# Performance work log

Hardware: AMD Instinct MI355X
Metric: run time of the kernel (lower is better)

## Reference

```python
import jax, jax.numpy as jnp
import numpy as np
import math

N_EMBD = 1024
N_HEAD = 16
BLOCK = 2048
B, T = 2, 2048


def setup_inputs() -> dict:
    key = jax.random.key(0)
    ks = jax.random.split(key, 5)
    s = 0.02
    return {
        "x": jax.random.normal(ks[0], (B, T, N_EMBD), dtype=jnp.float32),
        "W_attn": jax.random.normal(ks[1], (3 * N_EMBD, N_EMBD), dtype=jnp.float32) * s,  # [out,in] torch layout
        "b_attn": jax.random.normal(ks[2], (3 * N_EMBD,), dtype=jnp.float32) * s,
        "W_proj": jax.random.normal(ks[3], (N_EMBD, N_EMBD), dtype=jnp.float32) * s,
        "b_proj": jax.random.normal(ks[4], (N_EMBD,), dtype=jnp.float32) * s,
    }


def reference(x, W_attn, b_attn, W_proj, b_proj):
    Bx, Tx, C = x.shape
    H = N_HEAD
    D = C // H
    qkv = jnp.einsum("btc,oc->bto", x, W_attn) + b_attn  # [B,T,3C]
    q, k, v = jnp.split(qkv, 3, axis=-1)
    # [B,T,H,D] -> [B,H,T,D]
    q = q.reshape(Bx, Tx, H, D).transpose(0, 2, 1, 3)
    k = k.reshape(Bx, Tx, H, D).transpose(0, 2, 1, 3)
    v = v.reshape(Bx, Tx, H, D).transpose(0, 2, 1, 3)
    att = jnp.einsum("bhqd,bhkd->bhqk", q, k) * (1.0 / math.sqrt(D))
    causal = jnp.tril(jnp.ones((Tx, Tx), dtype=bool))
    att = jnp.where(causal[None, None], att, -jnp.inf)
    att = jax.nn.softmax(att, axis=-1)
    y = jnp.einsum("bhqk,bhkd->bhqd", att, v)  # [B,H,T,D]
    y = y.transpose(0, 2, 1, 3).reshape(Bx, Tx, C)
    y = jnp.einsum("btc,oc->bto", y, W_proj) + b_proj
    return y
```

## Files before the change

### kernel.cpp

```cpp
#include <hip/hip_runtime.h>
#include <hip/hip_bf16.h>
#include <stdint.h>

typedef unsigned short u16;
using f32x4 = __attribute__((ext_vector_type(4))) float;
using s16x8 = __attribute__((ext_vector_type(8))) short;

#define B_SZ 2
#define T_SZ 2048
#define C_SZ 1024
#define H_SZ 16
#define D_SZ 64

#define Q_SCALE 0.18033688011112042f

__device__ __forceinline__ u16 f2bf(float f) {
  __hip_bfloat16 h = __float2bfloat16(f);
  return *(u16*)&h;
}

__device__ __forceinline__ void async16(const u16* g, u16* l) {
  __builtin_amdgcn_global_load_lds((__attribute__((address_space(1))) void*)(g),
                                   (__attribute__((address_space(3))) void*)(l),
                                   16, 0, 0);
}

__global__ void cvt3_kernel(const float* __restrict__ a, int na,
                            const float* __restrict__ b, int nb,
                            const float* __restrict__ c, int nc,
                            u16* __restrict__ out) {
  int n = na + nb + nc;
  for (int i = blockIdx.x * blockDim.x + threadIdx.x; i < n; i += gridDim.x * blockDim.x) {
    const float* src; int off;
    if (i < na)           { src = a; off = i; }
    else if (i < na + nb) { src = b; off = i - na; }
    else                  { src = c; off = i - na - nb; }
    float4 v = reinterpret_cast<const float4*>(src)[off];
    ushort4 o;
    o.x = f2bf(v.x); o.y = f2bf(v.y); o.z = f2bf(v.z); o.w = f2bf(v.w);
    reinterpret_cast<ushort4*>(out)[i] = o;
  }
}

__global__ __launch_bounds__(256) void gemm_qkv(
    const u16* __restrict__ A, const u16* __restrict__ W,
    const float* __restrict__ bias,
    u16* __restrict__ Qo, u16* __restrict__ Ko, u16* __restrict__ Vt)
{
  const int K = 1024;
  const int NT = 32;
  __shared__ __align__(16) u16 lA[2][128 * 32];
  __shared__ __align__(16) u16 lB[2][128 * 32];
  int tid = threadIdx.x, lane = tid & 63, wave = tid >> 6;
  int wm = (wave >> 1) * 64, wn = (wave & 1) * 64;
  int bm = blockIdx.x * 128, bn = blockIdx.y * 128;
  int r = lane & 15, g = lane >> 4;

  int p0 = tid, p1 = 256 + tid;
  int ar0 = p0 >> 2, ar1 = p1 >> 2;
  int al0 = (p0 & 3) ^ (ar0 & 3), al1 = (p1 & 3) ^ (ar1 & 3);
  const u16* As0 = A + (size_t)(bm + ar0) * K + al0 * 8;
  const u16* As1 = A + (size_t)(bm + ar1) * K + al1 * 8;
  const u16* Ws0 = W + (size_t)(bn + ar0) * K + al0 * 8;
  const u16* Ws1 = W + (size_t)(bn + ar1) * K + al1 * 8;

  f32x4 acc[4][4];
#pragma unroll
  for (int i = 0; i < 4; ++i)
#pragma unroll
    for (int j = 0; j < 4; ++j)
      acc[i][j] = (f32x4){0.f, 0.f, 0.f, 0.f};

  int rd_off = r * 32 + ((g ^ (r & 3)) * 8);

  async16(As0, &lA[0][p0 * 8]);
  async16(As1, &lA[0][p1 * 8]);
  async16(Ws0, &lB[0][p0 * 8]);
  async16(Ws1, &lB[0][p1 * 8]);
  __syncthreads();

  int cur = 0;
  for (int t = 0; t < NT; ++t) {
    if (t + 1 < NT) {
      int k0 = (t + 1) * 32;
      int nb_ = cur ^ 1;
      async16(As0 + k0, &lA[nb_][p0 * 8]);
      async16(As1 + k0, &lA[nb_][p1 * 8]);
      async16(Ws0 + k0, &lB[nb_][p0 * 8]);
      async16(Ws1 + k0, &lB[nb_][p1 * 8]);
    }
    s16x8 af[4], bf[4];
#pragma unroll
    for (int i = 0; i < 4; ++i)
      af[i] = *(const s16x8*)(&lA[cur][(wm + i * 16) * 32 + rd_off]);
#pragma unroll
    for (int j = 0; j < 4; ++j)
      bf[j] = *(const s16x8*)(&lB[cur][(wn + j * 16) * 32 + rd_off]);
#pragma unroll
    for (int i = 0; i < 4; ++i)
#pragma unroll
      for (int j = 0; j < 4; ++j)
        acc[i][j] = __builtin_amdgcn_mfma_f32_16x16x32_bf16(af[i], bf[j], acc[i][j], 0, 0, 0);
    __syncthreads();
    cur ^= 1;
  }

  int seg = bn >> 10;
#pragma unroll
  for (int i = 0; i < 4; ++i) {
#pragma unroll
    for (int j = 0; j < 4; ++j) {
      int col = bn + wn + j * 16 + r;
      int cc = col & 1023;
      int h = cc >> 6, d = cc & 63;
      float bv = bias[col];
      int row0 = bm + wm + i * 16 + g * 4;
      int b = row0 >> 11, t0 = row0 & 2047;
      if (seg == 2) {
        ushort4 pv;
        pv.x = f2bf(acc[i][j][0] + bv);
        pv.y = f2bf(acc[i][j][1] + bv);
        pv.z = f2bf(acc[i][j][2] + bv);
        pv.w = f2bf(acc[i][j][3] + bv);
        *reinterpret_cast<ushort4*>(Vt + ((size_t)(b * H_SZ + h) * D_SZ + d) * T_SZ + t0) = pv;
      } else {
        u16* dst = (seg == 0) ? Qo : Ko;
        float scale = (seg == 0) ? Q_SCALE : 1.0f;
#pragma unroll
        for (int rr = 0; rr < 4; ++rr) {
          float v = (acc[i][j][rr] + bv) * scale;
          dst[(((size_t)(b * H_SZ + h) * T_SZ + (t0 + rr)) * D_SZ) + d] = f2bf(v);
        }
      }
    }
  }
}

__global__ __launch_bounds__(256) void gemm_proj(
    const u16* __restrict__ A, const u16* __restrict__ W,
    const float* __restrict__ bias, float* __restrict__ out)
{
  const int K = 1024;
  const int NT = 32;
  __shared__ __align__(16) u16 lA[2][128 * 32];
  __shared__ __align__(16) u16 lB[2][128 * 32];
  int tid = threadIdx.x, lane = tid & 63, wave = tid >> 6;
  int wm = (wave >> 1) * 64, wn = (wave & 1) * 64;
  int bm = blockIdx.x * 128, bn = blockIdx.y * 128;
  int r = lane & 15, g = lane >> 4;

  int p0 = tid, p1 = 256 + tid;
  int ar0 = p0 >> 2, ar1 = p1 >> 2;
  int al0 = (p0 & 3) ^ (ar0 & 3), al1 = (p1 & 3) ^ (ar1 & 3);
  const u16* As0 = A + (size_t)(bm + ar0) * K + al0 * 8;
  const u16* As1 = A + (size_t)(bm + ar1) * K + al1 * 8;
  const u16* Ws0 = W + (size_t)(bn + ar0) * K + al0 * 8;
  const u16* Ws1 = W + (size_t)(bn + ar1) * K + al1 * 8;

  f32x4 acc[4][4];
#pragma unroll
  for (int i = 0; i < 4; ++i)
#pragma unroll
    for (int j = 0; j < 4; ++j)
      acc[i][j] = (f32x4){0.f, 0.f, 0.f, 0.f};

  int rd_off = r * 32 + ((g ^ (r & 3)) * 8);

  async16(As0, &lA[0][p0 * 8]);
  async16(As1, &lA[0][p1 * 8]);
  async16(Ws0, &lB[0][p0 * 8]);
  async16(Ws1, &lB[0][p1 * 8]);
  __syncthreads();

  int cur = 0;
  for (int t = 0; t < NT; ++t) {
    if (t + 1 < NT) {
      int k0 = (t + 1) * 32;
      int nb_ = cur ^ 1;
      async16(As0 + k0, &lA[nb_][p0 * 8]);
      async16(As1 + k0, &lA[nb_][p1 * 8]);
      async16(Ws0 + k0, &lB[nb_][p0 * 8]);
      async16(Ws1 + k0, &lB[nb_][p1 * 8]);
    }
    s16x8 af[4], bf[4];
#pragma unroll
    for (int i = 0; i < 4; ++i)
      af[i] = *(const s16x8*)(&lA[cur][(wm + i * 16) * 32 + rd_off]);
#pragma unroll
    for (int j = 0; j < 4; ++j)
      bf[j] = *(const s16x8*)(&lB[cur][(wn + j * 16) * 32 + rd_off]);
#pragma unroll
    for (int i = 0; i < 4; ++i)
#pragma unroll
      for (int j = 0; j < 4; ++j)
        acc[i][j] = __builtin_amdgcn_mfma_f32_16x16x32_bf16(af[i], bf[j], acc[i][j], 0, 0, 0);
    __syncthreads();
    cur ^= 1;
  }

#pragma unroll
  for (int i = 0; i < 4; ++i) {
#pragma unroll
    for (int j = 0; j < 4; ++j) {
      int col = bn + wn + j * 16 + r;
      float bv = bias[col];
#pragma unroll
      for (int rr = 0; rr < 4; ++rr) {
        int row = bm + wm + i * 16 + g * 4 + rr;
        out[(size_t)row * 1024 + col] = acc[i][j][rr] + bv;
      }
    }
  }
}

__global__ __launch_bounds__(256) void attn_kernel(
    const u16* __restrict__ Q, const u16* __restrict__ K, const u16* __restrict__ Vt,
    u16* __restrict__ Y)
{
  __shared__ __align__(16) u16 lK[2][64 * 64];
  __shared__ __align__(16) u16 lV[2][64 * 64];
  __shared__ __align__(16) u16 lP[4][16 * 64];
  int tid = threadIdx.x, lane = tid & 63, wave = tid >> 6;
  int bh = blockIdx.x;
  int qt = 31 - blockIdx.y;
  const u16* Qh = Q + (size_t)bh * T_SZ * D_SZ;
  const u16* Kh = K + (size_t)bh * T_SZ * D_SZ;
  const u16* Vh = Vt + (size_t)bh * D_SZ * T_SZ;
  int r = lane & 15, g = lane >> 4;
  int wq = qt * 64 + wave * 16;
  int qrow = wq + r;

  s16x8 qf0 = *(const s16x8*)(Qh + (size_t)qrow * 64 + g * 8);
  s16x8 qf1 = *(const s16x8*)(Qh + (size_t)qrow * 64 + 32 + g * 8);

  int p0 = tid, p1 = 256 + tid;
  int r0 = p0 >> 3, r1 = p1 >> 3;
  int l0 = (p0 & 7) ^ (r0 & 7), l1 = (p1 & 7) ^ (r1 & 7);

  float s0 = 0.f, s1 = 0.f, s2 = 0.f, s3 = 0.f;
  f32x4 o[4];
#pragma unroll
  for (int j = 0; j < 4; ++j) o[j] = (f32x4){0.f, 0.f, 0.f, 0.f};

  u16* lPw = lP[wave];

  async16(Kh + (size_t)r0 * 64 + l0 * 8, &lK[0][p0 * 8]);
  async16(Kh + (size_t)r1 * 64 + l1 * 8, &lK[0][p1 * 8]);
  async16(Vh + (size_t)r0 * T_SZ + l0 * 8, &lV[0][p0 * 8]);
  async16(Vh + (size_t)r1 * T_SZ + l1 * 8, &lV[0][p1 * 8]);
  __syncthreads();

  int cur = 0;
  for (int kt = 0; kt <= qt; ++kt) {
    int kvbase = kt * 64;
    if (kt < qt) {
      int nb_ = cur ^ 1;
      int kb = kvbase + 64;
      async16(Kh + (size_t)(kb + r0) * 64 + l0 * 8, &lK[nb_][p0 * 8]);
      async16(Kh + (size_t)(kb + r1) * 64 + l1 * 8, &lK[nb_][p1 * 8]);
      async16(Vh + (size_t)r0 * T_SZ + kb + l0 * 8, &lV[nb_][p0 * 8]);
      async16(Vh + (size_t)r1 * T_SZ + kb + l1 * 8, &lV[nb_][p1 * 8]);
    }

    f32x4 sf[4];
    __builtin_amdgcn_s_setprio(1);
#pragma unroll
    for (int jj = 0; jj < 4; ++jj) {
      int krow = jj * 16 + r;
      const s16x8 kf0 = *(const s16x8*)(&lK[cur][krow * 64 + ((g ^ (r & 7)) * 8)]);
      const s16x8 kf1 = *(const s16x8*)(&lK[cur][krow * 64 + (((4 + g) ^ (r & 7)) * 8)]);
      f32x4 sv = (f32x4){0.f, 0.f, 0.f, 0.f};
      sv = __builtin_amdgcn_mfma_f32_16x16x32_bf16(kf0, qf0, sv, 0, 0, 0);
      sv = __builtin_amdgcn_mfma_f32_16x16x32_bf16(kf1, qf1, sv, 0, 0, 0);
      sf[jj] = sv;
    }
    __builtin_amdgcn_s_setprio(0);

    if (kt == qt) {
#pragma unroll
      for (int jj = 0; jj < 4; ++jj)
#pragma unroll
        for (int rr = 0; rr < 4; ++rr) {
          int kv = kvbase + jj * 16 + g * 4 + rr;
          sf[jj][rr] = (kv <= qrow) ? sf[jj][rr] : -3e30f;
        }
    }

#pragma unroll
    for (int jj = 0; jj < 4; ++jj) {
      float pv0 = __builtin_amdgcn_exp2f(sf[jj][0]);
      float pv1 = __builtin_amdgcn_exp2f(sf[jj][1]);
      float pv2 = __builtin_amdgcn_exp2f(sf[jj][2]);
      float pv3 = __builtin_amdgcn_exp2f(sf[jj][3]);
      s0 += pv0; s1 += pv1; s2 += pv2; s3 += pv3;
      ushort4 pk;
      pk.x = f2bf(pv0); pk.y = f2bf(pv1); pk.z = f2bf(pv2); pk.w = f2bf(pv3);
      int off = r * 64 + ((jj * 16 + 4 * g) ^ ((r & 7) << 3));
      *reinterpret_cast<ushort4*>(lPw + off) = pk;
    }

    __builtin_amdgcn_s_setprio(1);
#pragma unroll
    for (int hh = 0; hh < 2; ++hh) {
      const s16x8 pa = *(const s16x8*)(lPw + r * 64 + (((hh * 4 + g) ^ (r & 7)) * 8));
#pragma unroll
      for (int j = 0; j < 4; ++j) {
        int vrow = j * 16 + r;
        const s16x8 vb = *(const s16x8*)(&lV[cur][vrow * 64 + (((hh * 4 + g) ^ (r & 7)) * 8)]);
        o[j] = __builtin_amdgcn_mfma_f32_16x16x32_bf16(vb, pa, o[j], 0, 0, 0);
      }
    }
    __builtin_amdgcn_s_setprio(0);
    __syncthreads();
    cur ^= 1;
  }

  float s = (s0 + s1) + (s2 + s3);
  s += __shfl_xor(s, 16);
  s += __shfl_xor(s, 32);
  float sinv = 1.0f / s;
  int b = bh >> 4, h = bh & 15;
  size_t ybase = ((size_t)(b * T_SZ + qrow)) * C_SZ + h * 64;
#pragma unroll
  for (int j = 0; j < 4; ++j) {
    ushort4 pk;
    pk.x = f2bf(o[j][0] * sinv);
    pk.y = f2bf(o[j][1] * sinv);
    pk.z = f2bf(o[j][2] * sinv);
    pk.w = f2bf(o[j][3] * sinv);
    *reinterpret_cast<ushort4*>(Y + ybase + j * 16 + g * 4) = pk;
  }
}

extern "C" void kernel_launch(void* const* d_in, const int* in_sizes, int n_in,
                              void* d_out, int out_size, void* d_ws, size_t ws_size,
                              hipStream_t stream) {
  const float* x      = (const float*)d_in[0];
  const float* W_attn = (const float*)d_in[1];
  const float* b_attn = (const float*)d_in[2];
  const float* W_proj = (const float*)d_in[3];
  const float* b_proj = (const float*)d_in[4];
  float* out = (float*)d_out;

  char* ws = (char*)d_ws;
  u16* xb  = (u16*)ws; ws += (size_t)4096 * 1024 * 2;
  u16* wab = (u16*)ws; ws += (size_t)3072 * 1024 * 2;
  u16* wpb = (u16*)ws; ws += (size_t)1024 * 1024 * 2;
  u16* Qb  = (u16*)ws; ws += (size_t)B_SZ * H_SZ * T_SZ * D_SZ * 2;
  u16* Kb  = (u16*)ws; ws += (size_t)B_SZ * H_SZ * T_SZ * D_SZ * 2;
  u16* Vtb = (u16*)ws; ws += (size_t)B_SZ * H_SZ * T_SZ * D_SZ * 2;
  u16* Yb  = (u16*)ws; ws += (size_t)4096 * 1024 * 2;

  int n4x = 4096 * 1024 / 4;
  int n4a = 3072 * 1024 / 4;
  int n4p = 1024 * 1024 / 4;
  cvt3_kernel<<<2048, 256, 0, stream>>>(x, n4x, W_attn, n4a, W_proj, n4p, xb);

  gemm_qkv<<<dim3(32, 24), 256, 0, stream>>>(xb, wab, b_attn, Qb, Kb, Vtb);
  attn_kernel<<<dim3(32, 32), 256, 0, stream>>>(Qb, Kb, Vtb, Yb);
  gemm_proj<<<dim3(32, 8), 256, 0, stream>>>(Yb, wpb, b_proj, out);
}
```

Baseline: 111.7 us.

## Enlarge QKV GEMM tile to 256x256 with 4-stage async LDS pipeline

Rewrites the QKV projection GEMM to use 512-thread blocks computing 256x256 output tiles, with each wave holding an 8x4 block of MFMA fragments. The old double buffer becomes a 4-deep ring of LDS buffers filled three tiles ahead. Hand-written vmcnt waits and a single barrier per iteration replace the per-iteration __syncthreads, and the MFMA section runs at raised priority. The aim is more operand reuse and better overlap of global loads with compute. In exchange the grid shrinks to 192 blocks and each block uses 128KB of LDS, which may leave some CUs idle.

```diff
diff --git a/kernel.cpp b/kernel.cpp
--- a/kernel.cpp
+++ b/kernel.cpp
@@ -42,98 +42,106 @@
   }
 }
 
-__global__ __launch_bounds__(256) void gemm_qkv(
+__global__ __launch_bounds__(512, 2) void gemm_qkv(
     const u16* __restrict__ A, const u16* __restrict__ W,
     const float* __restrict__ bias,
     u16* __restrict__ Qo, u16* __restrict__ Ko, u16* __restrict__ Vt)
 {
   const int K = 1024;
   const int NT = 32;
-  __shared__ __align__(16) u16 lA[2][128 * 32];
-  __shared__ __align__(16) u16 lB[2][128 * 32];
-  int tid = threadIdx.x, lane = tid & 63, wave = tid >> 6;
-  int wm = (wave >> 1) * 64, wn = (wave & 1) * 64;
-  int bm = blockIdx.x * 128, bn = blockIdx.y * 128;
+  __shared__ __align__(16) u16 lA[4][256 * 32];
+  __shared__ __align__(16) u16 lB[4][256 * 32];
+  int tid = threadIdx.x, lane = tid & 63;
+  int wid = tid >> 6;
+  int wr = wid >> 2, wc = wid & 3;
+  int bm = blockIdx.x * 256, bn = blockIdx.y * 256;
   int r = lane & 15, g = lane >> 4;
 
-  int p0 = tid, p1 = 256 + tid;
-  int ar0 = p0 >> 2, ar1 = p1 >> 2;
-  int al0 = (p0 & 3) ^ (ar0 & 3), al1 = (p1 & 3) ^ (ar1 & 3);
+  int c0 = tid, c1 = 512 + tid;
+  int ar0 = c0 >> 2, ar1 = c1 >> 2;
+  int al0 = (c0 & 3) ^ (ar0 & 3), al1 = (c1 & 3) ^ (ar1 & 3);
   const u16* As0 = A + (size_t)(bm + ar0) * K + al0 * 8;
   const u16* As1 = A + (size_t)(bm + ar1) * K + al1 * 8;
   const u16* Ws0 = W + (size_t)(bn + ar0) * K + al0 * 8;
   const u16* Ws1 = W + (size_t)(bn + ar1) * K + al1 * 8;
 
-  f32x4 acc[4][4];
-#pragma unroll
-  for (int i = 0; i < 4; ++i)
+#define STAGE_QKV(buf, t) do { int k0_ = (t) * 32;          \
+    async16(As0 + k0_, &lA[buf][c0 * 8]);                   \
+    async16(As1 + k0_, &lA[buf][c1 * 8]);                   \
+    async16(Ws0 + k0_, &lB[buf][c0 * 8]);                   \
+    async16(Ws1 + k0_, &lB[buf][c1 * 8]); } while (0)
+
+  f32x4 acc[8][4];
+#pragma unroll
+  for (int i = 0; i < 8; ++i)
 #pragma unroll
     for (int j = 0; j < 4; ++j)
       acc[i][j] = (f32x4){0.f, 0.f, 0.f, 0.f};
 
-  int rd_off = r * 32 + ((g ^ (r & 3)) * 8);
-
-  async16(As0, &lA[0][p0 * 8]);
-  async16(As1, &lA[0][p1 * 8]);
-  async16(Ws0, &lB[0][p0 * 8]);
-  async16(Ws1, &lB[0][p1 * 8]);
-  __syncthreads();
-
-  int cur = 0;
+  int kchunk = (g ^ (r & 3)) * 8;
+  int abase = (wr * 128 + r) * 32 + kchunk;
+  int bbase = (wc * 64 + r) * 32 + kchunk;
+
+  STAGE_QKV(0, 0);
+  STAGE_QKV(1, 1);
+  STAGE_QKV(2, 2);
+
   for (int t = 0; t < NT; ++t) {
-    if (t + 1 < NT) {
-      int k0 = (t + 1) * 32;
-      int nb_ = cur ^ 1;
-      async16(As0 + k0, &lA[nb_][p0 * 8]);
-      async16(As1 + k0, &lA[nb_][p1 * 8]);
-      async16(Ws0 + k0, &lB[nb_][p0 * 8]);
-      async16(Ws1 + k0, &lB[nb_][p1 * 8]);
-    }
-    s16x8 af[4], bf[4];
-#pragma unroll
-    for (int i = 0; i < 4; ++i)
-      af[i] = *(const s16x8*)(&lA[cur][(wm + i * 16) * 32 + rd_off]);
-#pragma unroll
-    for (int j = 0; j < 4; ++j)
-      bf[j] = *(const s16x8*)(&lB[cur][(wn + j * 16) * 32 + rd_off]);
-#pragma unroll
-    for (int i = 0; i < 4; ++i)
-#pragma unroll
-      for (int j = 0; j < 4; ++j)
-        acc[i][j] = __builtin_amdgcn_mfma_f32_16x16x32_bf16(af[i], bf[j], acc[i][j], 0, 0, 0);
-    __syncthreads();
-    cur ^= 1;
+    if (t < NT - 2)       asm volatile("s_waitcnt vmcnt(8)" ::: "memory");
+    else if (t == NT - 2) asm volatile("s_waitcnt vmcnt(4)" ::: "memory");
+    else                  asm volatile("s_waitcnt vmcnt(0)" ::: "memory");
+    __builtin_amdgcn_s_barrier();
+    if (t + 3 < NT) STAGE_QKV((t + 3) & 3, t + 3);
+
+    const u16* a_ = lA[t & 3];
+    const u16* b_ = lB[t & 3];
+    s16x8 af[8], bf[4];
+#pragma unroll
+    for (int mf = 0; mf < 8; ++mf)
+      af[mf] = *(const s16x8*)(a_ + abase + mf * 16 * 32);
+#pragma unroll
+    for (int nf = 0; nf < 4; ++nf)
+      bf[nf] = *(const s16x8*)(b_ + bbase + nf * 16 * 32);
+
+    __builtin_amdgcn_s_setprio(1);
+#pragma unroll
+    for (int mf = 0; mf < 8; ++mf)
+#pragma unroll
+      for (int nf = 0; nf < 4; ++nf)
+        acc[mf][nf] = __builtin_amdgcn_mfma_f32_16x16x32_bf16(af[mf], bf[nf], acc[mf][nf], 0, 0, 0);
+    __builtin_amdgcn_s_setprio(0);
   }
 
   int seg = bn >> 10;
 #pragma unroll
-  for (int i = 0; i < 4; ++i) {
-#pragma unroll
-    for (int j = 0; j < 4; ++j) {
-      int col = bn + wn + j * 16 + r;
-      int cc = col & 1023;
-      int h = cc >> 6, d = cc & 63;
-      float bv = bias[col];
-      int row0 = bm + wm + i * 16 + g * 4;
+  for (int nf = 0; nf < 4; ++nf) {
+    int col = bn + wc * 64 + nf * 16 + r;
+    int cc = col & 1023;
+    int h = cc >> 6, d = cc & 63;
+    float bv = bias[col];
+#pragma unroll
+    for (int mf = 0; mf < 8; ++mf) {
+      int row0 = bm + wr * 128 + mf * 16 + g * 4;
       int b = row0 >> 11, t0 = row0 & 2047;
       if (seg == 2) {
         ushort4 pv;
-        pv.x = f2bf(acc[i][j][0] + bv);
-        pv.y = f2bf(acc[i][j][1] + bv);
-        pv.z = f2bf(acc[i][j][2] + bv);
-        pv.w = f2bf(acc[i][j][3] + bv);
+        pv.x = f2bf(acc[mf][nf][0] + bv);
+        pv.y = f2bf(acc[mf][nf][1] + bv);
+        pv.z = f2bf(acc[mf][nf][2] + bv);
+        pv.w = f2bf(acc[mf][nf][3] + bv);
         *reinterpret_cast<ushort4*>(Vt + ((size_t)(b * H_SZ + h) * D_SZ + d) * T_SZ + t0) = pv;
       } else {
         u16* dst = (seg == 0) ? Qo : Ko;
         float scale = (seg == 0) ? Q_SCALE : 1.0f;
 #pragma unroll
         for (int rr = 0; rr < 4; ++rr) {
-          float v = (acc[i][j][rr] + bv) * scale;
+          float v = (acc[mf][nf][rr] + bv) * scale;
           dst[(((size_t)(b * H_SZ + h) * T_SZ + (t0 + rr)) * D_SZ) + d] = f2bf(v);
         }
       }
     }
   }
+#undef STAGE_QKV
 }
 
 __global__ __launch_bounds__(256) void gemm_proj(
@@ -356,7 +364,7 @@
   int n4p = 1024 * 1024 / 4;
   cvt3_kernel<<<2048, 256, 0, stream>>>(x, n4x, W_attn, n4a, W_proj, n4p, xb);
 
-  gemm_qkv<<<dim3(32, 24), 256, 0, stream>>>(xb, wab, b_attn, Qb, Kb, Vtb);
+  gemm_qkv<<<dim3(16, 12), 512, 0, stream>>>(xb, wab, b_attn, Qb, Kb, Vtb);
   attn_kernel<<<dim3(32, 32), 256, 0, stream>>>(Qb, Kb, Vtb, Yb);
   gemm_proj<<<dim3(32, 8), 256, 0, stream>>>(Yb, wpb, b_proj, out);
 }
```

Result: slower. 121.0 us (+8.3%).

## Process two 16-row query sub-tiles per wave to reuse K/V tiles

Applied to the files above, without the earlier changes.

Each attention block now covers 128 query rows instead of 64, with each wave holding two 16-row query fragments and two output accumulators. Every K/V tile loaded into LDS feeds twice as many MFMAs, which halves the global K/V traffic and the block count. The cost is more registers per wave and fewer blocks (512 instead of 1024), which lowers occupancy and coarsens the causal load balance. The diagonal-masking condition is widened to cover the last two KV tiles. The P buffer in LDS is reused in sequence for both sub-tiles.

```diff
diff --git a/kernel.cpp b/kernel.cpp
--- a/kernel.cpp
+++ b/kernel.cpp
@@ -222,27 +222,35 @@
   __shared__ __align__(16) u16 lP[4][16 * 64];
   int tid = threadIdx.x, lane = tid & 63, wave = tid >> 6;
   int bh = blockIdx.x;
-  int qt = 31 - blockIdx.y;
+  int qb = 15 - blockIdx.y;
   const u16* Qh = Q + (size_t)bh * T_SZ * D_SZ;
   const u16* Kh = K + (size_t)bh * T_SZ * D_SZ;
   const u16* Vh = Vt + (size_t)bh * D_SZ * T_SZ;
   int r = lane & 15, g = lane >> 4;
-  int wq = qt * 64 + wave * 16;
-  int qrow = wq + r;
-
-  s16x8 qf0 = *(const s16x8*)(Qh + (size_t)qrow * 64 + g * 8);
-  s16x8 qf1 = *(const s16x8*)(Qh + (size_t)qrow * 64 + 32 + g * 8);
+  int wq = qb * 128 + wave * 32;
+  int qrow0 = wq + r;
+  int qrow1 = wq + 16 + r;
+
+  s16x8 qf00 = *(const s16x8*)(Qh + (size_t)qrow0 * 64 + g * 8);
+  s16x8 qf01 = *(const s16x8*)(Qh + (size_t)qrow0 * 64 + 32 + g * 8);
+  s16x8 qf10 = *(const s16x8*)(Qh + (size_t)qrow1 * 64 + g * 8);
+  s16x8 qf11 = *(const s16x8*)(Qh + (size_t)qrow1 * 64 + 32 + g * 8);
 
   int p0 = tid, p1 = 256 + tid;
   int r0 = p0 >> 3, r1 = p1 >> 3;
   int l0 = (p0 & 7) ^ (r0 & 7), l1 = (p1 & 7) ^ (r1 & 7);
 
-  float s0 = 0.f, s1 = 0.f, s2 = 0.f, s3 = 0.f;
-  f32x4 o[4];
-#pragma unroll
-  for (int j = 0; j < 4; ++j) o[j] = (f32x4){0.f, 0.f, 0.f, 0.f};
+  f32x4 ssum0 = (f32x4){0.f, 0.f, 0.f, 0.f};
+  f32x4 ssum1 = (f32x4){0.f, 0.f, 0.f, 0.f};
+  f32x4 o0[4], o1[4];
+#pragma unroll
+  for (int j = 0; j < 4; ++j) {
+    o0[j] = (f32x4){0.f, 0.f, 0.f, 0.f};
+    o1[j] = (f32x4){0.f, 0.f, 0.f, 0.f};
+  }
 
   u16* lPw = lP[wave];
+  const int NT = 2 * qb + 2;
 
   async16(Kh + (size_t)r0 * 64 + l0 * 8, &lK[0][p0 * 8]);
   async16(Kh + (size_t)r1 * 64 + l1 * 8, &lK[0][p1 * 8]);
@@ -251,9 +259,9 @@
   __syncthreads();
 
   int cur = 0;
-  for (int kt = 0; kt <= qt; ++kt) {
+  for (int kt = 0; kt < NT; ++kt) {
     int kvbase = kt * 64;
-    if (kt < qt) {
+    if (kt + 1 < NT) {
       int nb_ = cur ^ 1;
       int kb = kvbase + 64;
       async16(Kh + (size_t)(kb + r0) * 64 + l0 * 8, &lK[nb_][p0 * 8]);
@@ -262,7 +270,7 @@
       async16(Vh + (size_t)r1 * T_SZ + kb + l1 * 8, &lV[nb_][p1 * 8]);
     }
 
-    f32x4 sf[4];
+    f32x4 sf0[4], sf1[4];
     __builtin_amdgcn_s_setprio(1);
 #pragma unroll
     for (int jj = 0; jj < 4; ++jj) {
@@ -270,29 +278,34 @@
       const s16x8 kf0 = *(const s16x8*)(&lK[cur][krow * 64 + ((g ^ (r & 7)) * 8)]);
       const s16x8 kf1 = *(const s16x8*)(&lK[cur][krow * 64 + (((4 + g) ^ (r & 7)) * 8)]);
       f32x4 sv = (f32x4){0.f, 0.f, 0.f, 0.f};
-      sv = __builtin_amdgcn_mfma_f32_16x16x32_bf16(kf0, qf0, sv, 0, 0, 0);
-      sv = __builtin_amdgcn_mfma_f32_16x16x32_bf16(kf1, qf1, sv, 0, 0, 0);
-      sf[jj] = sv;
+      sv = __builtin_amdgcn_mfma_f32_16x16x32_bf16(kf0, qf00, sv, 0, 0, 0);
+      sv = __builtin_amdgcn_mfma_f32_16x16x32_bf16(kf1, qf01, sv, 0, 0, 0);
+      sf0[jj] = sv;
+      f32x4 sw = (f32x4){0.f, 0.f, 0.f, 0.f};
+      sw = __builtin_amdgcn_mfma_f32_16x16x32_bf16(kf0, qf10, sw, 0, 0, 0);
+      sw = __builtin_amdgcn_mfma_f32_16x16x32_bf16(kf1, qf11, sw, 0, 0, 0);
+      sf1[jj] = sw;
     }
     __builtin_amdgcn_s_setprio(0);
 
-    if (kt == qt) {
+    if (kt >= 2 * qb) {
 #pragma unroll
       for (int jj = 0; jj < 4; ++jj)
 #pragma unroll
         for (int rr = 0; rr < 4; ++rr) {
           int kv = kvbase + jj * 16 + g * 4 + rr;
-          sf[jj][rr] = (kv <= qrow) ? sf[jj][rr] : -3e30f;
+          sf0[jj][rr] = (kv <= qrow0) ? sf0[jj][rr] : -3e30f;
+          sf1[jj][rr] = (kv <= qrow1) ? sf1[jj][rr] : -3e30f;
         }
     }
 
 #pragma unroll
     for (int jj = 0; jj < 4; ++jj) {
-      float pv0 = __builtin_amdgcn_exp2f(sf[jj][0]);
-      float pv1 = __builtin_amdgcn_exp2f(sf[jj][1]);
-      float pv2 = __builtin_amdgcn_exp2f(sf[jj][2]);
-      float pv3 = __builtin_amdgcn_exp2f(sf[jj][3]);
-      s0 += pv0; s1 += pv1; s2 += pv2; s3 += pv3;
+      float pv0 = __builtin_amdgcn_exp2f(sf0[jj][0]);
+      float pv1 = __builtin_amdgcn_exp2f(sf0[jj][1]);
+      float pv2 = __builtin_amdgcn_exp2f(sf0[jj][2]);
+      float pv3 = __builtin_amdgcn_exp2f(sf0[jj][3]);
+      ssum0[0] += pv0; ssum0[1] += pv1; ssum0[2] += pv2; ssum0[3] += pv3;
       ushort4 pk;
       pk.x = f2bf(pv0); pk.y = f2bf(pv1); pk.z = f2bf(pv2); pk.w = f2bf(pv3);
       int off = r * 64 + ((jj * 16 + 4 * g) ^ ((r & 7) << 3));
@@ -307,7 +320,33 @@
       for (int j = 0; j < 4; ++j) {
         int vrow = j * 16 + r;
         const s16x8 vb = *(const s16x8*)(&lV[cur][vrow * 64 + (((hh * 4 + g) ^ (r & 7)) * 8)]);
-        o[j] = __builtin_amdgcn_mfma_f32_16x16x32_bf16(vb, pa, o[j], 0, 0, 0);
+        o0[j] = __builtin_amdgcn_mfma_f32_16x16x32_bf16(vb, pa, o0[j], 0, 0, 0);
+      }
+    }
+    __builtin_amdgcn_s_setprio(0);
+
+#pragma unroll
+    for (int jj = 0; jj < 4; ++jj) {
+      float pv0 = __builtin_amdgcn_exp2f(sf1[jj][0]);
+      float pv1 = __builtin_amdgcn_exp2f(sf1[jj][1]);
+      float pv2 = __builtin_amdgcn_exp2f(sf1[jj][2]);
+      float pv3 = __builtin_amdgcn_exp2f(sf1[jj][3]);
+      ssum1[0] += pv0; ssum1[1] += pv1; ssum1[2] += pv2; ssum1[3] += pv3;
+      ushort4 pk;
+      pk.x = f2bf(pv0); pk.y = f2bf(pv1); pk.z = f2bf(pv2); pk.w = f2bf(pv3);
+      int off = r * 64 + ((jj * 16 + 4 * g) ^ ((r & 7) << 3));
+      *reinterpret_cast<ushort4*>(lPw + off) = pk;
+    }
+
+    __builtin_amdgcn_s_setprio(1);
+#pragma unroll
+    for (int hh = 0; hh < 2; ++hh) {
+      const s16x8 pa = *(const s16x8*)(lPw + r * 64 + (((hh * 4 + g) ^ (r & 7)) * 8));
+#pragma unroll
+      for (int j = 0; j < 4; ++j) {
+        int vrow = j * 16 + r;
+        const s16x8 vb = *(const s16x8*)(&lV[cur][vrow * 64 + (((hh * 4 + g) ^ (r & 7)) * 8)]);
+        o1[j] = __builtin_amdgcn_mfma_f32_16x16x32_bf16(vb, pa, o1[j], 0, 0, 0);
       }
     }
     __builtin_amdgcn_s_setprio(0);
@@ -315,20 +354,38 @@
     cur ^= 1;
   }
 
-  float s = (s0 + s1) + (s2 + s3);
-  s += __shfl_xor(s, 16);
-  s += __shfl_xor(s, 32);
-  float sinv = 1.0f / s;
   int b = bh >> 4, h = bh & 15;
-  size_t ybase = ((size_t)(b * T_SZ + qrow)) * C_SZ + h * 64;
-#pragma unroll
-  for (int j = 0; j < 4; ++j) {
-    ushort4 pk;
-    pk.x = f2bf(o[j][0] * sinv);
-    pk.y = f2bf(o[j][1] * sinv);
-    pk.z = f2bf(o[j][2] * sinv);
-    pk.w = f2bf(o[j][3] * sinv);
-    *reinterpret_cast<ushort4*>(Y + ybase + j * 16 + g * 4) = pk;
+  {
+    float s = (ssum0[0] + ssum0[1]) + (ssum0[2] + ssum0[3]);
+    s += __shfl_xor(s, 16);
+    s += __shfl_xor(s, 32);
+    float sinv = 1.0f / s;
+    size_t ybase = ((size_t)(b * T_SZ + qrow0)) * C_SZ + h * 64;
+#pragma unroll
+    for (int j = 0; j < 4; ++j) {
+      ushort4 pk;
+      pk.x = f2bf(o0[j][0] * sinv);
+      pk.y = f2bf(o0[j][1] * sinv);
+      pk.z = f2bf(o0[j][2] * sinv);
+      pk.w = f2bf(o0[j][3] * sinv);
+      *reinterpret_cast<ushort4*>(Y + ybase + j * 16 + g * 4) = pk;
+    }
+  }
+  {
+    float s = (ssum1[0] + ssum1[1]) + (ssum1[2] + ssum1[3]);
+    s += __shfl_xor(s, 16);
+    s += __shfl_xor(s, 32);
+    float sinv = 1.0f / s;
+    size_t ybase = ((size_t)(b * T_SZ + qrow1)) * C_SZ + h * 64;
+#pragma unroll
+    for (int j = 0; j < 4; ++j) {
+      ushort4 pk;
+      pk.x = f2bf(o1[j][0] * sinv);
+      pk.y = f2bf(o1[j][1] * sinv);
+      pk.z = f2bf(o1[j][2] * sinv);
+      pk.w = f2bf(o1[j][3] * sinv);
+      *reinterpret_cast<ushort4*>(Y + ybase + j * 16 + g * 4) = pk;
+    }
   }
 }
 
@@ -357,6 +414,6 @@
   cvt3_kernel<<<2048, 256, 0, stream>>>(x, n4x, W_attn, n4a, W_proj, n4p, xb);
 
   gemm_qkv<<<dim3(32, 24), 256, 0, stream>>>(xb, wab, b_attn, Qb, Kb, Vtb);
-  attn_kernel<<<dim3(32, 32), 256, 0, stream>>>(Qb, Kb, Vtb, Yb);
+  attn_kernel<<<dim3(32, 16), 256, 0, stream>>>(Qb, Kb, Vtb, Yb);
   gemm_proj<<<dim3(32, 8), 256, 0, stream>>>(Yb, wpb, b_proj, out);
 }
```

Measured after the change: 125.1 us. +11.9%, slower.

## Enlarge attention query tile to 128 rows with 8 waves per block

Applied to the files above, without the earlier changes.

The attention kernel now uses 512 threads (8 waves), each block covering 128 query rows, so every K/V tile staged in LDS is shared by twice as many waves and half as many blocks reload it. Query blocks are scheduled in a paired order, heavy tiles first and then light ones, to balance the causal workload. Each block's KV loop now runs to the end of its 128-row range, so the first 64-row half of each block computes one extra, fully masked KV tile, and waves in that half mask both diagonal tiles. The change halves the grid to 512 blocks, which may reduce occupancy and parallelism.

```diff
diff --git a/kernel.cpp b/kernel.cpp
--- a/kernel.cpp
+++ b/kernel.cpp
@@ -213,29 +213,30 @@
   }
 }
 
-__global__ __launch_bounds__(256) void attn_kernel(
+__global__ __launch_bounds__(512) void attn_kernel(
     const u16* __restrict__ Q, const u16* __restrict__ K, const u16* __restrict__ Vt,
     u16* __restrict__ Y)
 {
   __shared__ __align__(16) u16 lK[2][64 * 64];
   __shared__ __align__(16) u16 lV[2][64 * 64];
-  __shared__ __align__(16) u16 lP[4][16 * 64];
+  __shared__ __align__(16) u16 lP[8][16 * 64];
   int tid = threadIdx.x, lane = tid & 63, wave = tid >> 6;
   int bh = blockIdx.x;
-  int qt = 31 - blockIdx.y;
+  int by = blockIdx.y;
+  int qb = (by < 8) ? (15 - by) : (by - 8);
   const u16* Qh = Q + (size_t)bh * T_SZ * D_SZ;
   const u16* Kh = K + (size_t)bh * T_SZ * D_SZ;
   const u16* Vh = Vt + (size_t)bh * D_SZ * T_SZ;
   int r = lane & 15, g = lane >> 4;
-  int wq = qt * 64 + wave * 16;
+  int wq = qb * 128 + wave * 16;
   int qrow = wq + r;
+  int tdiag = wq >> 6;
 
   s16x8 qf0 = *(const s16x8*)(Qh + (size_t)qrow * 64 + g * 8);
   s16x8 qf1 = *(const s16x8*)(Qh + (size_t)qrow * 64 + 32 + g * 8);
 
-  int p0 = tid, p1 = 256 + tid;
-  int r0 = p0 >> 3, r1 = p1 >> 3;
-  int l0 = (p0 & 7) ^ (r0 & 7), l1 = (p1 & 7) ^ (r1 & 7);
+  int srow = tid >> 3;
+  int slc = (tid & 7) ^ (srow & 7);
 
   float s0 = 0.f, s1 = 0.f, s2 = 0.f, s3 = 0.f;
   f32x4 o[4];
@@ -243,23 +244,20 @@
   for (int j = 0; j < 4; ++j) o[j] = (f32x4){0.f, 0.f, 0.f, 0.f};
 
   u16* lPw = lP[wave];
-
-  async16(Kh + (size_t)r0 * 64 + l0 * 8, &lK[0][p0 * 8]);
-  async16(Kh + (size_t)r1 * 64 + l1 * 8, &lK[0][p1 * 8]);
-  async16(Vh + (size_t)r0 * T_SZ + l0 * 8, &lV[0][p0 * 8]);
-  async16(Vh + (size_t)r1 * T_SZ + l1 * 8, &lV[0][p1 * 8]);
+  const int NT = 2 * qb + 2;
+
+  async16(Kh + (size_t)srow * 64 + slc * 8, &lK[0][tid * 8]);
+  async16(Vh + (size_t)srow * T_SZ + slc * 8, &lV[0][tid * 8]);
   __syncthreads();
 
   int cur = 0;
-  for (int kt = 0; kt <= qt; ++kt) {
+  for (int kt = 0; kt < NT; ++kt) {
     int kvbase = kt * 64;
-    if (kt < qt) {
+    if (kt + 1 < NT) {
       int nb_ = cur ^ 1;
       int kb = kvbase + 64;
-      async16(Kh + (size_t)(kb + r0) * 64 + l0 * 8, &lK[nb_][p0 * 8]);
-      async16(Kh + (size_t)(kb + r1) * 64 + l1 * 8, &lK[nb_][p1 * 8]);
-      async16(Vh + (size_t)r0 * T_SZ + kb + l0 * 8, &lV[nb_][p0 * 8]);
-      async16(Vh + (size_t)r1 * T_SZ + kb + l1 * 8, &lV[nb_][p1 * 8]);
+      async16(Kh + (size_t)(kb + srow) * 64 + slc * 8, &lK[nb_][tid * 8]);
+      async16(Vh + (size_t)srow * T_SZ + kb + slc * 8, &lV[nb_][tid * 8]);
     }
 
     f32x4 sf[4];
@@ -276,7 +274,7 @@
     }
     __builtin_amdgcn_s_setprio(0);
 
-    if (kt == qt) {
+    if (kt >= tdiag) {
 #pragma unroll
       for (int jj = 0; jj < 4; ++jj)
 #pragma unroll
@@ -357,6 +355,6 @@
   cvt3_kernel<<<2048, 256, 0, stream>>>(x, n4x, W_attn, n4a, W_proj, n4p, xb);
 
   gemm_qkv<<<dim3(32, 24), 256, 0, stream>>>(xb, wab, b_attn, Qb, Kb, Vtb);
-  attn_kernel<<<dim3(32, 32), 256, 0, stream>>>(Qb, Kb, Vtb, Yb);
+  attn_kernel<<<dim3(32, 16), 512, 0, stream>>>(Qb, Kb, Vtb, Yb);
   gemm_proj<<<dim3(32, 8), 256, 0, stream>>>(Yb, wpb, b_proj, out);
 }
```

Measured after the change: 114.8 us. 1.03x slower.
